# Performance work log

Hardware: AMD Instinct MI355X
Metric: run time of the kernel (lower is better)

Reference implementation:

```python
import jax, jax.numpy as jnp
import numpy as np

BITS = 4
QMAX = 2 ** (BITS - 1) - 1   # 7
OFF = 2 ** (BITS - 1)        # 8
L = 2 ** BITS                # 16 LUT levels per operand


def _quant(x):
    """Symmetric per-tensor quantization to signed BITS-bit levels.
    Returns integer-valued levels (as float, in [-OFF, QMAX]) and the scale."""
    s = jnp.maximum(jnp.max(jnp.abs(x)) / QMAX, 1e-8)
    q = jnp.clip(jnp.round(x / s), -OFF, QMAX)
    return q, s


def _lut_conv3x3(x, w, b, lut):
    """3x3 same-padding conv where every scalar multiply a*w is replaced by
    lut[idx(a), idx(w)]. x:[B,C,H,W], w:[O,C,3,3], b:[O], lut:[L,L]."""
    B, C, H, W = x.shape
    O = w.shape[0]
    qx, sx = _quant(x)
    qw, sw = _quant(w)
    # zero-padding: level 0 is the quantized value 0, so padding is exact
    xp = jnp.pad(qx, ((0, 0), (0, 0), (1, 1), (1, 1)))
    # im2col: [B, C, 9, H, W] -> [B, H, W, K], K = C*9 (order: c-major, then kh,kw)
    patches = jnp.stack([xp[:, :, i:i + H, j:j + W]
                         for i in range(3) for j in range(3)], axis=2)
    K = C * 9
    patches = patches.reshape(B, K, H, W).transpose(0, 2, 3, 1)
    idx_a = (patches + OFF).astype(jnp.int32)            # [B,H,W,K]
    mapped = lut[idx_a]                                   # [B,H,W,K,L]
    idx_w = (qw.reshape(O, K).T + OFF).astype(jnp.int32)  # [K,O]
    onehot_w = jax.nn.one_hot(idx_w, L, dtype=x.dtype)    # [K,O,L]
    # out[b,o,h,w] = sum_k lut[idx_a[b,h,w,k], idx_w[k,o]]
    out = jnp.einsum('bhwkl,kol->bohw', mapped, onehot_w)
    return out * (sx * sw) + b[None, :, None, None]


def _lut_linear(x, w, b, lut):
    """x:[B,F], w:[O,F], b:[O], lut:[L,L]; y[b,o]=sum_f lut[idx(x),idx(w)]."""
    qx, sx = _quant(x)
    qw, sw = _quant(w)
    idx_a = (qx + OFF).astype(jnp.int32)                 # [B,F]
    mapped = lut[idx_a]                                   # [B,F,L]
    idx_w = (qw.T + OFF).astype(jnp.int32)                # [F,O]
    onehot_w = jax.nn.one_hot(idx_w, L, dtype=x.dtype)    # [F,O,L]
    out = jnp.einsum('bfl,fol->bo', mapped, onehot_w)
    return out * (sx * sw) + b[None, :]


def _maxpool2(x):
    B, C, H, W = x.shape
    return x.reshape(B, C, H // 2, 2, W // 2, 2).max(axis=(3, 5))


def setup_inputs() -> dict:
    key = jax.random.key(0)
    ks = jax.random.split(key, 20)
    d = {}
    d['x'] = jax.random.normal(ks[0], (8, 3, 32, 32), jnp.float32)
    conv_shapes = [(64, 3), (192, 64), (384, 192), (256, 384), (256, 256)]
    for i, (o, c) in enumerate(conv_shapes):
        d[f'w{i}'] = jax.random.normal(ks[1 + 2 * i], (o, c, 3, 3), jnp.float32) * 0.05
        d[f'b{i}'] = jax.random.normal(ks[2 + 2 * i], (o,), jnp.float32) * 0.01
    fc_shapes = [(4096, 4096), (4096, 4096), (10, 4096)]
    for j, (o, f) in enumerate(fc_shapes):
        d[f'w{5 + j}'] = jax.random.normal(ks[11 + 2 * j], (o, f), jnp.float32) * 0.02
        d[f'b{5 + j}'] = jax.random.normal(ks[12 + 2 * j], (o,), jnp.float32) * 0.01
    # per-layer approximate-multiplier LUTs: exact product of signed levels + error
    levels = jnp.arange(-OFF, OFF, dtype=jnp.float32)       # [-8..7]
    base = jnp.outer(levels, levels)                        # [16,16]
    noise = jax.random.normal(ks[17], (8, L, L), jnp.float32) * 0.25
    d['luts'] = base[None, :, :] + noise
    return d


def reference(x, w0, b0, w1, b1, w2, b2, w3, b3, w4, b4,
              w5, b5, w6, b6, w7, b7, luts):
    relu = jax.nn.relu
    h = relu(_lut_conv3x3(x, w0, b0, luts[0]))
    h = _maxpool2(h)                                  # [B,64,16,16]
    h = relu(_lut_conv3x3(h, w1, b1, luts[1]))
    h = _maxpool2(h)                                  # [B,192,8,8]
    h = relu(_lut_conv3x3(h, w2, b2, luts[2]))        # [B,384,8,8]
    h = relu(_lut_conv3x3(h, w3, b3, luts[3]))        # [B,256,8,8]
    h = relu(_lut_conv3x3(h, w4, b4, luts[4]))
    h = _maxpool2(h)                                  # [B,256,4,4]
    h = h.reshape(h.shape[0], 256 * 4 * 4)
    h = relu(_lut_linear(h, w5, b5, luts[5]))         # dropout = identity (eval)
    h = relu(_lut_linear(h, w6, b6, luts[6]))
    return _lut_linear(h, w7, b7, luts[7])            # [B,10]
```

## Files before the change

kernel.cpp:

```cpp
#include <hip/hip_runtime.h>
#include <stdint.h>


#define DI __device__ __forceinline__

constexpr size_t alup(size_t x){ return (x + 511) & ~(size_t)511; }
constexpr size_t O_SLOTS = 0;
constexpr size_t O_IA0 = 512;
constexpr size_t O_IA1 = alup(O_IA0 + 24576);
constexpr size_t O_IA2 = alup(O_IA1 + 131072);
constexpr size_t O_IA3 = alup(O_IA2 + 98304);
constexpr size_t O_IA4 = alup(O_IA3 + 196608);
constexpr size_t O_IA5 = alup(O_IA4 + 131072);
constexpr size_t O_IA6 = alup(O_IA5 + 32768);
constexpr size_t O_IA7 = alup(O_IA6 + 32768);
constexpr size_t O_WP0 = alup(O_IA7 + 32768);
constexpr size_t O_WP1 = alup(O_WP0 + 864);
constexpr size_t O_WP2 = alup(O_WP1 + 55296);
constexpr size_t O_WP3 = alup(O_WP2 + 331776);
constexpr size_t O_WP4 = alup(O_WP3 + 442368);
constexpr size_t O_A1  = alup(O_WP4 + 294912);
constexpr size_t O_A2  = alup(O_A1 + 1048576);
constexpr size_t O_A3  = alup(O_A2 + 786432);
constexpr size_t O_A4  = alup(O_A3 + 1572864);
constexpr size_t O_A5  = alup(O_A4 + 1048576);
constexpr size_t O_H5  = alup(O_A5 + 262144);
constexpr size_t O_H6  = alup(O_H5 + 262144);
constexpr size_t O_P1  = alup(O_H6 + 262144);
constexpr size_t O_P2  = O_P1 + 3145728;
constexpr size_t O_P3  = O_P2 + 1572864;
constexpr size_t O_P4  = O_P3 + 1048576;
constexpr int    PZ_D4 = 212992;


DI double getscale(const double* slots, int i){ return fmax(slots[i] / 7.0, 1e-8); }
DI int quant_idx_r(double v, double r){
  double q = fmin(fmax(rint(v * r), -8.0), 7.0);
  return (int)q + 8;
}
DI void atomicMaxD(double* addr, double v){
  atomicMax((unsigned long long*)addr, (unsigned long long)__double_as_longlong(v));
}

__global__ __launch_bounds__(256) void k_zero_all(double4* pz, double* slots){
  int i = blockIdx.x*256 + threadIdx.x;
  if (i < PZ_D4){ double4 z; z.x=z.y=z.z=z.w=0.0; pz[i] = z; }
  else if (i - PZ_D4 < 16) slots[i - PZ_D4] = 0.0;
}

__global__ __launch_bounds__(256) void k_wmax(
    const float* w0, const float* w1, const float* w2, const float* w3, const float* w4,
    const float* w5, const float* w6, const float* w7, const float* x, double* slots)
{
  const int sizes[9] = {1728,110592,663552,884736,589824,16777216,16777216,40960,24576};
  const int cum[10]  = {0,1,5,26,53,71,583,1095,1097,1098};
  int bid = blockIdx.x;
  int seg = 0;
  #pragma unroll
  for (int s2 = 0; s2 < 9; ++s2) if (bid >= cum[s2+1]) seg = s2+1;
  const float* p;
  switch (seg){
    case 0: p = w0; break; case 1: p = w1; break; case 2: p = w2; break;
    case 3: p = w3; break; case 4: p = w4; break; case 5: p = w5; break;
    case 6: p = w6; break; case 7: p = w7; break; default: p = x; break;
  }
  int n = sizes[seg];
  long base = (long)(bid - cum[seg]) * 32768;
  float m = 0.f;
  for (long i = base + threadIdx.x * 4; i < base + 32768 && i < (long)n; i += 1024){
    float4 v = *(const float4*)(p + i);
    m = fmaxf(m, fmaxf(fmaxf(fabsf(v.x), fabsf(v.y)), fmaxf(fabsf(v.z), fabsf(v.w))));
  }
  #pragma unroll
  for (int off = 32; off; off >>= 1) m = fmaxf(m, __shfl_xor(m, off, 64));
  __shared__ float red[4];
  if ((threadIdx.x & 63) == 0) red[threadIdx.x >> 6] = m;
  __syncthreads();
  if (threadIdx.x == 0)
    atomicMaxD(&slots[seg], (double)fmaxf(fmaxf(red[0], red[1]), fmaxf(red[2], red[3])));
}

__global__ __launch_bounds__(256) void k_wq(
    const float* w0, const float* w1, const float* w2, const float* w3, const float* w4,
    const float* x, const double* slots, uint8_t* ws)
{
  int item = blockIdx.x * 256 + threadIdx.x;
  if (item < 281304){
    const float* w; uint32_t* wp; int K; int r; double s;
    if (item < 216)        { w=w0; wp=(uint32_t*)(ws+O_WP0); K=27;   r=item;        s=getscale(slots,0); }
    else if (item < 14040) { w=w1; wp=(uint32_t*)(ws+O_WP1); K=576;  r=item-216;    s=getscale(slots,1); }
    else if (item < 96984) { w=w2; wp=(uint32_t*)(ws+O_WP2); K=1728; r=item-14040;  s=getscale(slots,2); }
    else if (item < 207576){ w=w3; wp=(uint32_t*)(ws+O_WP3); K=3456; r=item-96984;  s=getscale(slots,3); }
    else                   { w=w4; wp=(uint32_t*)(ws+O_WP4); K=2304; r=item-207576; s=getscale(slots,4); }
    double rs = 1.0 / s;
    int og = r / K, k = r % K;
    uint32_t pack = 0;
    #pragma unroll
    for (int j = 0; j < 8; ++j){
      double wv = (double)w[(size_t)(og*8 + j)*K + k];
      pack |= (uint32_t)quant_idx_r(wv, rs) << (4*j);
    }
    wp[og*K + k] = pack;
  } else if (item < 287448){
    int i2 = item - 281304;
    double rs = 1.0 / getscale(slots, 8);
    uint32_t pack = 0;
    #pragma unroll
    for (int r2 = 0; r2 < 4; ++r2)
      pack |= (uint32_t)quant_idx_r((double)x[i2*4 + r2], rs) << (8*r2);
    ((uint32_t*)(ws + O_IA0))[i2] = pack;
  }
}

__global__ __launch_bounds__(256) void k_conv0(
    const uint8_t* __restrict__ ia0, const uint32_t* __restrict__ wp0,
    const float* __restrict__ lut_g, const float* __restrict__ bias,
    double* slots, double* __restrict__ a1)
{
  __shared__ double lutT[256];
  int tid = threadIdx.x;
  lutT[(tid & 15)*16 + (tid >> 4)] = (double)lut_g[tid];
  __syncthreads();
  int b = blockIdx.x >> 6, o = blockIdx.x & 63;
  int yp = tid >> 4, xp = tid & 15;
  double scale = getscale(slots, 8) * getscale(slots, 0);
  double bo = (double)bias[o];
  double pool = 0.0;
  #pragma unroll
  for (int dy = 0; dy < 2; ++dy)
  #pragma unroll
  for (int dx = 0; dx < 2; ++dx){
    int y = yp*2 + dy, x2 = xp*2 + dx;
    double sum = 0.0;
    #pragma unroll
    for (int c = 0; c < 3; ++c)
      #pragma unroll
      for (int ty = 0; ty < 3; ++ty)
        #pragma unroll
        for (int tx = 0; tx < 3; ++tx){
          int yy = y + ty - 1, xx = x2 + tx - 1;
          int ia = 8;
          if (yy >= 0 && yy < 32 && xx >= 0 && xx < 32)
            ia = ia0[((b*3 + c)*32 + yy)*32 + xx];
          uint32_t sw = wp0[(o >> 3)*27 + c*9 + ty*3 + tx];
          int iw = (sw >> ((o & 7)*4)) & 15;
          sum += lutT[iw*16 + ia];
        }
    pool = fmax(pool, fmax(sum*scale + bo, 0.0));
  }
  a1[((b*64 + o)*16 + yp)*16 + xp] = pool;
  double m = pool;
  #pragma unroll
  for (int off = 32; off; off >>= 1) m = fmax(m, __shfl_xor(m, off, 64));
  __shared__ double red[4];
  if ((tid & 63) == 0) red[tid >> 6] = m;
  __syncthreads();
  if (tid == 0) atomicMaxD(&slots[9], fmax(fmax(red[0],red[1]), fmax(red[2],red[3])));
}

template<int C, int O, int H, int W, int CT, int ROWS, int SP, int KS>
__global__ __launch_bounds__(256) void k_conv(
    const uint8_t* __restrict__ iain, const uint32_t* __restrict__ wp,
    const float* __restrict__ lut_g, double* __restrict__ P)
{
  constexpr int KT = CT*9;
  constexpr int AW = W + 2, AH = ROWS + 2;
  __shared__ double lutT[256];
  __shared__ uint32_t wps[4*KT];
  __shared__ uint8_t acts[CT*AH*AW];
  int tid = threadIdx.x;
  int bx = blockIdx.x;
  int ks = bx % KS; int rem = bx / KS;
  int ob = rem % (O/32); rem /= (O/32);
  int sp = rem % SP; int b = rem / SP;
  lutT[(tid & 15)*16 + (tid >> 4)] = (double)lut_g[tid];
  for (int i = tid; i < 4*KT; i += 256){
    int w2 = i / KT, k = i % KT;
    wps[i] = wp[(size_t)(ob*4 + w2)*(C*9) + (size_t)ks*KT + k];
  }
  for (int i = tid; i < CT*AH*AW; i += 256){
    int ct = i / (AH*AW);
    int r  = (i / AW) % AH;
    int cc = i % AW;
    int y = sp*ROWS + r - 1, x2 = cc - 1;
    uint8_t v = 8;
    if (y >= 0 && y < H && x2 >= 0 && x2 < W)
      v = iain[(((size_t)b*C + ks*CT + ct)*H + y)*W + x2];
    acts[i] = v;
  }
  __syncthreads();
  int wid = tid >> 6, lane = tid & 63;
  int ly = lane / W, lx = lane % W;
  double acc[8] = {0,0,0,0,0,0,0,0};
  const uint32_t* wrow = &wps[wid*KT];
  #pragma unroll 1
  for (int ct = 0; ct < CT; ++ct){
    int abase = (ct*AH + ly)*AW + lx;
    #pragma unroll
    for (int ty = 0; ty < 3; ++ty)
    #pragma unroll
    for (int tx = 0; tx < 3; ++tx){
      int ia = acts[abase + ty*AW + tx];
      uint32_t sw = (uint32_t)__builtin_amdgcn_readfirstlane((int)wrow[ct*9 + ty*3 + tx]);
      #pragma unroll
      for (int j = 0; j < 8; ++j)
        acc[j] += lutT[((sw >> (4*j)) & 15u)*16 + ia];
    }
  }
  int y = sp*ROWS + ly;
  int obase = ob*32 + wid*8;
  #pragma unroll
  for (int j = 0; j < 8; ++j)
    atomicAdd(&P[(((size_t)b*O + obase + j)*H + y)*W + lx], acc[j]);
}

template<int O, int Hc, int Wc, bool POOL>
__global__ __launch_bounds__(256) void k_post(
    const double* __restrict__ P, const float* __restrict__ bias,
    double* __restrict__ aout, double* slots, int sx_slot, int sw_slot, int ma_slot)
{
  constexpr int Ho = POOL ? Hc/2 : Hc, Wo = POOL ? Wc/2 : Wc;
  int i = blockIdx.x*256 + threadIdx.x;
  int x2 = i % Wo, y = (i / Wo) % Ho, o = (i / (Wo*Ho)) % O, b = i / (Wo*Ho*O);
  double scale = getscale(slots, sx_slot) * getscale(slots, sw_slot);
  double bo = (double)bias[o];
  double res;
  if (POOL){
    double p = 0.0;
    #pragma unroll
    for (int dy = 0; dy < 2; ++dy)
    #pragma unroll
    for (int dx = 0; dx < 2; ++dx){
      double s = P[(((size_t)b*O + o)*Hc + y*2+dy)*Wc + x2*2+dx];
      p = fmax(p, fmax(s*scale + bo, 0.0));
    }
    res = p;
  } else {
    double s = P[(((size_t)b*O + o)*Hc + y)*Wc + x2];
    res = fmax(s*scale + bo, 0.0);
  }
  aout[i] = res;
  double m = res;
  #pragma unroll
  for (int off = 32; off; off >>= 1) m = fmax(m, __shfl_xor(m, off, 64));
  __shared__ double red[4];
  if ((threadIdx.x & 63) == 0) red[threadIdx.x >> 6] = m;
  __syncthreads();
  if (threadIdx.x == 0)
    atomicMaxD(&slots[ma_slot], fmax(fmax(red[0],red[1]), fmax(red[2],red[3])));
}

__global__ __launch_bounds__(256) void k_aq_conv(
    const double* __restrict__ in, uint8_t* __restrict__ out,
    const double* slots, int slot, int n)
{
  int i = blockIdx.x*256 + threadIdx.x;
  if (i >= n) return;
  double rs = 1.0 / getscale(slots, slot);
  out[i] = (uint8_t)quant_idx_r(in[i], rs);
}

__global__ __launch_bounds__(256) void k_aq_fc(
    const double* __restrict__ in, uint32_t* __restrict__ lo, uint32_t* __restrict__ hi,
    const double* slots, int slot)
{
  int f = blockIdx.x*256 + threadIdx.x;
  double rs = 1.0 / getscale(slots, slot);
  uint32_t l = 0, h = 0;
  #pragma unroll
  for (int b2 = 0; b2 < 4; ++b2) l |= (uint32_t)quant_idx_r(in[(size_t)b2*4096 + f], rs) << (8*b2);
  #pragma unroll
  for (int b2 = 4; b2 < 8; ++b2) h |= (uint32_t)quant_idx_r(in[(size_t)b2*4096 + f], rs) << (8*(b2-4));
  lo[f] = l; hi[f] = h;
}

template<bool RELU>
__global__ __launch_bounds__(256) void k_fc(
    const float* __restrict__ Wm, const float* __restrict__ bias,
    const uint32_t* __restrict__ ialo, const uint32_t* __restrict__ iahi,
    const float* __restrict__ lut_g, double* __restrict__ out,
    double* slots, int sx_slot, int sw_slot, int ma_slot)
{
  __shared__ double lutT[256];
  __shared__ uint32_t los[4096], his[4096];
  __shared__ double red[4];
  int tid = threadIdx.x;
  lutT[(tid & 15)*16 + (tid >> 4)] = (double)lut_g[tid];
  for (int i = tid; i < 4096; i += 256){ los[i] = ialo[i]; his[i] = iahi[i]; }
  __syncthreads();
  double sw = getscale(slots, sw_slot);
  double rsw = 1.0 / sw;
  double scale = getscale(slots, sx_slot) * sw;
  int wid = tid >> 6, lane = tid & 63;
  int o = blockIdx.x*4 + wid;
  const float* wr = Wm + (size_t)o*4096;
  double acc[8] = {0,0,0,0,0,0,0,0};
  #pragma unroll 2
  for (int ch = 0; ch < 64; ++ch){
    int f = ch*64 + lane;
    unsigned iw = (unsigned)quant_idx_r((double)wr[f], rsw);
    const double* lrow = &lutT[iw << 4];
    uint32_t lo = los[f], hi = his[f];
    acc[0] += lrow[lo & 255];         acc[1] += lrow[(lo >> 8) & 255];
    acc[2] += lrow[(lo >> 16) & 255]; acc[3] += lrow[lo >> 24];
    acc[4] += lrow[hi & 255];         acc[5] += lrow[(hi >> 8) & 255];
    acc[6] += lrow[(hi >> 16) & 255]; acc[7] += lrow[hi >> 24];
  }
  #pragma unroll
  for (int off = 32; off; off >>= 1)
    #pragma unroll
    for (int b2 = 0; b2 < 8; ++b2) acc[b2] += __shfl_xor(acc[b2], off, 64);
  if (lane == 0){
    double m = 0.0;
    double bo = (double)bias[o];
    #pragma unroll
    for (int b2 = 0; b2 < 8; ++b2){
      double h = acc[b2]*scale + bo;
      if (RELU) h = fmax(h, 0.0);
      out[(size_t)b2*4096 + o] = h;
      m = fmax(m, fabs(h));
    }
    red[wid] = m;
  }
  __syncthreads();
  if (tid == 0)
    atomicMaxD(&slots[ma_slot], fmax(fmax(red[0],red[1]), fmax(red[2],red[3])));
}

__global__ __launch_bounds__(256) void k_fc7(
    const float* __restrict__ Wm, const float* __restrict__ bias,
    const uint32_t* __restrict__ ialo, const uint32_t* __restrict__ iahi,
    const float* __restrict__ lut_g, float* __restrict__ out, const double* slots)
{
  __shared__ double lutT[256];
  __shared__ uint32_t los[4096], his[4096];
  __shared__ double red[4][8];
  int tid = threadIdx.x;
  lutT[(tid & 15)*16 + (tid >> 4)] = (double)lut_g[tid];
  for (int i = tid; i < 4096; i += 256){ los[i] = ialo[i]; his[i] = iahi[i]; }
  __syncthreads();
  double sw = getscale(slots, 7);
  double rsw = 1.0 / sw;
  double scale = getscale(slots, 15) * sw;
  int o = blockIdx.x;
  const float* wr = Wm + (size_t)o*4096;
  double acc[8] = {0,0,0,0,0,0,0,0};
  for (int ch = 0; ch < 16; ++ch){
    int f = ch*256 + tid;
    unsigned iw = (unsigned)quant_idx_r((double)wr[f], rsw);
    const double* lrow = &lutT[iw << 4];
    uint32_t lo = los[f], hi = his[f];
    acc[0] += lrow[lo & 255];         acc[1] += lrow[(lo >> 8) & 255];
    acc[2] += lrow[(lo >> 16) & 255]; acc[3] += lrow[lo >> 24];
    acc[4] += lrow[hi & 255];         acc[5] += lrow[(hi >> 8) & 255];
    acc[6] += lrow[(hi >> 16) & 255]; acc[7] += lrow[hi >> 24];
  }
  int wid = tid >> 6, lane = tid & 63;
  #pragma unroll
  for (int off = 32; off; off >>= 1)
    #pragma unroll
    for (int b2 = 0; b2 < 8; ++b2) acc[b2] += __shfl_xor(acc[b2], off, 64);
  if (lane == 0){
    #pragma unroll
    for (int b2 = 0; b2 < 8; ++b2) red[wid][b2] = acc[b2];
  }
  __syncthreads();
  if (tid < 8){
    double v = red[0][tid] + red[1][tid] + red[2][tid] + red[3][tid];
    out[tid*10 + o] = (float)(v*scale + (double)bias[o]);
  }
}

extern "C" void kernel_launch(void* const* d_in, const int* in_sizes, int n_in,
                              void* d_out, int out_size, void* d_ws, size_t ws_size,
                              hipStream_t stream)
{
  (void)in_sizes; (void)n_in; (void)out_size; (void)ws_size;
  const float* x  = (const float*)d_in[0];
  const float* w0 = (const float*)d_in[1];  const float* b0 = (const float*)d_in[2];
  const float* w1 = (const float*)d_in[3];  const float* b1 = (const float*)d_in[4];
  const float* w2 = (const float*)d_in[5];  const float* b2 = (const float*)d_in[6];
  const float* w3 = (const float*)d_in[7];  const float* b3 = (const float*)d_in[8];
  const float* w4 = (const float*)d_in[9];  const float* b4 = (const float*)d_in[10];
  const float* w5 = (const float*)d_in[11]; const float* b5 = (const float*)d_in[12];
  const float* w6 = (const float*)d_in[13]; const float* b6 = (const float*)d_in[14];
  const float* w7 = (const float*)d_in[15]; const float* b7 = (const float*)d_in[16];
  const float* luts = (const float*)d_in[17];

  uint8_t* ws = (uint8_t*)d_ws;
  double* slots = (double*)(ws + O_SLOTS);
  const uint8_t* IA0 = ws + O_IA0;
  uint8_t *IA1 = ws + O_IA1, *IA2 = ws + O_IA2, *IA3 = ws + O_IA3, *IA4 = ws + O_IA4;
  uint32_t *IA5lo = (uint32_t*)(ws + O_IA5), *IA5hi = IA5lo + 4096;
  uint32_t *IA6lo = (uint32_t*)(ws + O_IA6), *IA6hi = IA6lo + 4096;
  uint32_t *IA7lo = (uint32_t*)(ws + O_IA7), *IA7hi = IA7lo + 4096;
  const uint32_t* WP0 = (const uint32_t*)(ws + O_WP0);
  const uint32_t* WP1 = (const uint32_t*)(ws + O_WP1);
  const uint32_t* WP2 = (const uint32_t*)(ws + O_WP2);
  const uint32_t* WP3 = (const uint32_t*)(ws + O_WP3);
  const uint32_t* WP4 = (const uint32_t*)(ws + O_WP4);
  double *A1 = (double*)(ws + O_A1), *A2 = (double*)(ws + O_A2), *A3 = (double*)(ws + O_A3);
  double *A4 = (double*)(ws + O_A4), *A5 = (double*)(ws + O_A5);
  double *H5 = (double*)(ws + O_H5), *H6 = (double*)(ws + O_H6);
  double *P1 = (double*)(ws + O_P1), *P2 = (double*)(ws + O_P2);
  double *P3 = (double*)(ws + O_P3), *P4 = (double*)(ws + O_P4);

  k_zero_all<<<833, 256, 0, stream>>>((double4*)(ws + O_P1), slots);
  k_wmax<<<1098, 256, 0, stream>>>(w0,w1,w2,w3,w4,w5,w6,w7,x,slots);
  k_wq<<<1123, 256, 0, stream>>>(w0,w1,w2,w3,w4,x,slots,ws);

  k_conv0<<<512, 256, 0, stream>>>(IA0, WP0, luts + 0, b0, slots, A1);
  k_aq_conv<<<512, 256, 0, stream>>>(A1, IA1, slots, 9, 131072);

  k_conv<64,192,16,16,8,4,4,8><<<1536, 256, 0, stream>>>(IA1, WP1, luts + 256, P1);
  k_post<192,16,16,true><<<384, 256, 0, stream>>>(P1, b1, A2, slots, 9, 1, 10);
  k_aq_conv<<<384, 256, 0, stream>>>(A2, IA2, slots, 10, 98304);

  k_conv<192,384,8,8,12,8,1,16><<<1536, 256, 0, stream>>>(IA2, WP2, luts + 512, P2);
  k_post<384,8,8,false><<<768, 256, 0, stream>>>(P2, b2, A3, slots, 10, 2, 11);
  k_aq_conv<<<768, 256, 0, stream>>>(A3, IA3, slots, 11, 196608);

  k_conv<384,256,8,8,12,8,1,32><<<2048, 256, 0, stream>>>(IA3, WP3, luts + 768, P3);
  k_post<256,8,8,false><<<512, 256, 0, stream>>>(P3, b3, A4, slots, 11, 3, 12);
  k_aq_conv<<<512, 256, 0, stream>>>(A4, IA4, slots, 12, 131072);

  k_conv<256,256,8,8,8,8,1,32><<<2048, 256, 0, stream>>>(IA4, WP4, luts + 1024, P4);
  k_post<256,8,8,true><<<128, 256, 0, stream>>>(P4, b4, A5, slots, 12, 4, 13);
  k_aq_fc<<<16, 256, 0, stream>>>(A5, IA5lo, IA5hi, slots, 13);

  k_fc<true><<<1024, 256, 0, stream>>>(w5, b5, IA5lo, IA5hi, luts + 1280, H5, slots, 13, 5, 14);
  k_aq_fc<<<16, 256, 0, stream>>>(H5, IA6lo, IA6hi, slots, 14);
  k_fc<true><<<1024, 256, 0, stream>>>(w6, b6, IA6lo, IA6hi, luts + 1536, H6, slots, 14, 6, 15);
  k_aq_fc<<<16, 256, 0, stream>>>(H6, IA7lo, IA7hi, slots, 15);
  k_fc7<<<10, 256, 0, stream>>>(w7, b7, IA7lo, IA7hi, luts + 1792, (float*)d_out, slots);
}
```

Before: 503.0 us.

## Fuse activation quantization into conv kernels and process batch pairs with pair LUT

Removes the separate activation-quantization kernels by quantizing the double activations on the fly inside each conv block. Each block now covers 8 output channels across all batch elements, with two batch samples packed into one byte. A 4096-entry float2 pair table serves both samples with one LDS read, and it is indexed through an XOR encoding so two samples with the same level share an entry. conv0 also stages its input tile in shared memory. The catch is that every conv block builds a 32KB shared table and re-quantizes overlapping input, and the LUT values are now accumulated from float rather than double.

```diff
diff --git a/kernel.cpp b/kernel.cpp
--- a/kernel.cpp
+++ b/kernel.cpp
@@ -7,11 +7,7 @@
 constexpr size_t alup(size_t x){ return (x + 511) & ~(size_t)511; }
 constexpr size_t O_SLOTS = 0;
 constexpr size_t O_IA0 = 512;
-constexpr size_t O_IA1 = alup(O_IA0 + 24576);
-constexpr size_t O_IA2 = alup(O_IA1 + 131072);
-constexpr size_t O_IA3 = alup(O_IA2 + 98304);
-constexpr size_t O_IA4 = alup(O_IA3 + 196608);
-constexpr size_t O_IA5 = alup(O_IA4 + 131072);
+constexpr size_t O_IA5 = alup(O_IA0 + 24576);
 constexpr size_t O_IA6 = alup(O_IA5 + 32768);
 constexpr size_t O_IA7 = alup(O_IA6 + 32768);
 constexpr size_t O_WP0 = alup(O_IA7 + 32768);
@@ -118,10 +114,12 @@
     double* slots, double* __restrict__ a1)
 {
   __shared__ double lutT[256];
+  __shared__ uint8_t xs[3072];
   int tid = threadIdx.x;
   lutT[(tid & 15)*16 + (tid >> 4)] = (double)lut_g[tid];
-  __syncthreads();
   int b = blockIdx.x >> 6, o = blockIdx.x & 63;
+  for (int i = tid; i < 3072; i += 256) xs[i] = ia0[b*3072 + i];
+  __syncthreads();
   int yp = tid >> 4, xp = tid & 15;
   double scale = getscale(slots, 8) * getscale(slots, 0);
   double bo = (double)bias[o];
@@ -141,7 +139,7 @@
           int yy = y + ty - 1, xx = x2 + tx - 1;
           int ia = 8;
           if (yy >= 0 && yy < 32 && xx >= 0 && xx < 32)
-            ia = ia0[((b*3 + c)*32 + yy)*32 + xx];
+            ia = xs[(c*32 + yy)*32 + xx];
           uint32_t sw = wp0[(o >> 3)*27 + c*9 + ty*3 + tx];
           int iw = (sw >> ((o & 7)*4)) & 15;
           sum += lutT[iw*16 + ia];
@@ -159,59 +157,75 @@
 }
 
 template<int C, int O, int H, int W, int CT, int ROWS, int SP, int KS>
-__global__ __launch_bounds__(256) void k_conv(
-    const uint8_t* __restrict__ iain, const uint32_t* __restrict__ wp,
-    const float* __restrict__ lut_g, double* __restrict__ P)
+__global__ __launch_bounds__(256) void k_convQ(
+    const double* __restrict__ Ain, const uint32_t* __restrict__ wp,
+    const float* __restrict__ lut_g, const double* __restrict__ slots, int slot,
+    double* __restrict__ P)
 {
   constexpr int KT = CT*9;
   constexpr int AW = W + 2, AH = ROWS + 2;
-  __shared__ double lutT[256];
-  __shared__ uint32_t wps[4*KT];
-  __shared__ uint8_t acts[CT*AH*AW];
+  __shared__ float2 pairT[4096];
+  __shared__ uint32_t wps[KT];
+  __shared__ uint8_t actsC[4*CT*AH*AW];
   int tid = threadIdx.x;
   int bx = blockIdx.x;
   int ks = bx % KS; int rem = bx / KS;
-  int ob = rem % (O/32); rem /= (O/32);
-  int sp = rem % SP; int b = rem / SP;
-  lutT[(tid & 15)*16 + (tid >> 4)] = (double)lut_g[tid];
-  for (int i = tid; i < 4*KT; i += 256){
-    int w2 = i / KT, k = i % KT;
-    wps[i] = wp[(size_t)(ob*4 + w2)*(C*9) + (size_t)ks*KT + k];
-  }
-  for (int i = tid; i < CT*AH*AW; i += 256){
-    int ct = i / (AH*AW);
-    int r  = (i / AW) % AH;
-    int cc = i % AW;
+  int ob = rem % (O/8); int sp = rem / (O/8);
+  for (int e = tid; e < 4096; e += 256){
+    int iw = e >> 8, s8 = e & 255;
+    int a1 = s8 >> 4, a2 = (s8 & 15) ^ a1;
+    pairT[e] = make_float2(lut_g[a1*16 + iw], lut_g[a2*16 + iw]);
+  }
+  for (int i = tid; i < KT; i += 256)
+    wps[i] = wp[(size_t)ob*(C*9) + ks*KT + i];
+  double rs = 1.0 / getscale(slots, slot);
+  constexpr int ATOT = 4*CT*AH*AW;
+  for (int i = tid; i < ATOT; i += 256){
+    int p2 = i / (CT*AH*AW);
+    int r2 = i % (CT*AH*AW);
+    int ct = r2 / (AH*AW);
+    int r = (r2 / AW) % AH;
+    int cc = r2 % AW;
     int y = sp*ROWS + r - 1, x2 = cc - 1;
-    uint8_t v = 8;
-    if (y >= 0 && y < H && x2 >= 0 && x2 < W)
-      v = iain[(((size_t)b*C + ks*CT + ct)*H + y)*W + x2];
-    acts[i] = v;
-  }
-  __syncthreads();
-  int wid = tid >> 6, lane = tid & 63;
+    uint8_t v = 136;
+    if (y >= 0 && y < H && x2 >= 0 && x2 < W){
+      size_t base = ((size_t)(2*p2)*C + ks*CT + ct)*H*W + (size_t)y*W + x2;
+      int q1 = quant_idx_r(Ain[base], rs);
+      int q2 = quant_idx_r(Ain[base + (size_t)C*H*W], rs);
+      v = (uint8_t)((q1 << 4) | q2);
+    }
+    actsC[i] = v;
+  }
+  __syncthreads();
+  int p = tid >> 6, lane = tid & 63;
   int ly = lane / W, lx = lane % W;
-  double acc[8] = {0,0,0,0,0,0,0,0};
-  const uint32_t* wrow = &wps[wid*KT];
+  double acc0[8] = {0,0,0,0,0,0,0,0};
+  double acc1[8] = {0,0,0,0,0,0,0,0};
   #pragma unroll 1
   for (int ct = 0; ct < CT; ++ct){
-    int abase = (ct*AH + ly)*AW + lx;
+    int abase = ((p*CT + ct)*AH + ly)*AW + lx;
     #pragma unroll
     for (int ty = 0; ty < 3; ++ty)
     #pragma unroll
     for (int tx = 0; tx < 3; ++tx){
-      int ia = acts[abase + ty*AW + tx];
-      uint32_t sw = (uint32_t)__builtin_amdgcn_readfirstlane((int)wrow[ct*9 + ty*3 + tx]);
+      int c = actsC[abase + ty*AW + tx];
+      int sl = c ^ (c >> 4);
+      uint32_t sw = (uint32_t)__builtin_amdgcn_readfirstlane((int)wps[ct*9 + ty*3 + tx]);
       #pragma unroll
-      for (int j = 0; j < 8; ++j)
-        acc[j] += lutT[((sw >> (4*j)) & 15u)*16 + ia];
+      for (int j = 0; j < 8; ++j){
+        float2 v = pairT[(((sw >> (4*j)) & 15u) << 8) + sl];
+        acc0[j] += (double)v.x;
+        acc1[j] += (double)v.y;
+      }
     }
   }
   int y = sp*ROWS + ly;
-  int obase = ob*32 + wid*8;
-  #pragma unroll
-  for (int j = 0; j < 8; ++j)
-    atomicAdd(&P[(((size_t)b*O + obase + j)*H + y)*W + lx], acc[j]);
+  #pragma unroll
+  for (int j = 0; j < 8; ++j){
+    size_t base = (((size_t)(2*p)*O + ob*8 + j)*H + y)*W + lx;
+    atomicAdd(&P[base], acc0[j]);
+    atomicAdd(&P[base + (size_t)O*H*W], acc1[j]);
+  }
 }
 
 template<int O, int Hc, int Wc, bool POOL>
@@ -248,16 +262,6 @@
   __syncthreads();
   if (threadIdx.x == 0)
     atomicMaxD(&slots[ma_slot], fmax(fmax(red[0],red[1]), fmax(red[2],red[3])));
-}
-
-__global__ __launch_bounds__(256) void k_aq_conv(
-    const double* __restrict__ in, uint8_t* __restrict__ out,
-    const double* slots, int slot, int n)
-{
-  int i = blockIdx.x*256 + threadIdx.x;
-  if (i >= n) return;
-  double rs = 1.0 / getscale(slots, slot);
-  out[i] = (uint8_t)quant_idx_r(in[i], rs);
 }
 
 __global__ __launch_bounds__(256) void k_aq_fc(
@@ -390,7 +394,6 @@
   uint8_t* ws = (uint8_t*)d_ws;
   double* slots = (double*)(ws + O_SLOTS);
   const uint8_t* IA0 = ws + O_IA0;
-  uint8_t *IA1 = ws + O_IA1, *IA2 = ws + O_IA2, *IA3 = ws + O_IA3, *IA4 = ws + O_IA4;
   uint32_t *IA5lo = (uint32_t*)(ws + O_IA5), *IA5hi = IA5lo + 4096;
   uint32_t *IA6lo = (uint32_t*)(ws + O_IA6), *IA6hi = IA6lo + 4096;
   uint32_t *IA7lo = (uint32_t*)(ws + O_IA7), *IA7hi = IA7lo + 4096;
@@ -410,21 +413,17 @@
   k_wq<<<1123, 256, 0, stream>>>(w0,w1,w2,w3,w4,x,slots,ws);
 
   k_conv0<<<512, 256, 0, stream>>>(IA0, WP0, luts + 0, b0, slots, A1);
-  k_aq_conv<<<512, 256, 0, stream>>>(A1, IA1, slots, 9, 131072);
-
-  k_conv<64,192,16,16,8,4,4,8><<<1536, 256, 0, stream>>>(IA1, WP1, luts + 256, P1);
+
+  k_convQ<64,192,16,16,4,4,4,16><<<1536, 256, 0, stream>>>(A1, WP1, luts + 256, slots, 9, P1);
   k_post<192,16,16,true><<<384, 256, 0, stream>>>(P1, b1, A2, slots, 9, 1, 10);
-  k_aq_conv<<<384, 256, 0, stream>>>(A2, IA2, slots, 10, 98304);
-
-  k_conv<192,384,8,8,12,8,1,16><<<1536, 256, 0, stream>>>(IA2, WP2, luts + 512, P2);
+
+  k_convQ<192,384,8,8,6,8,1,32><<<1536, 256, 0, stream>>>(A2, WP2, luts + 512, slots, 10, P2);
   k_post<384,8,8,false><<<768, 256, 0, stream>>>(P2, b2, A3, slots, 10, 2, 11);
-  k_aq_conv<<<768, 256, 0, stream>>>(A3, IA3, slots, 11, 196608);
-
-  k_conv<384,256,8,8,12,8,1,32><<<2048, 256, 0, stream>>>(IA3, WP3, luts + 768, P3);
+
+  k_convQ<384,256,8,8,8,8,1,48><<<1536, 256, 0, stream>>>(A3, WP3, luts + 768, slots, 11, P3);
   k_post<256,8,8,false><<<512, 256, 0, stream>>>(P3, b3, A4, slots, 11, 3, 12);
-  k_aq_conv<<<512, 256, 0, stream>>>(A4, IA4, slots, 12, 131072);
-
-  k_conv<256,256,8,8,8,8,1,32><<<2048, 256, 0, stream>>>(IA4, WP4, luts + 1024, P4);
+
+  k_convQ<256,256,8,8,4,8,1,64><<<2048, 256, 0, stream>>>(A4, WP4, luts + 1024, slots, 12, P4);
   k_post<256,8,8,true><<<128, 256, 0, stream>>>(P4, b4, A5, slots, 12, 4, 13);
   k_aq_fc<<<16, 256, 0, stream>>>(A5, IA5lo, IA5hi, slots, 13);
 
```

Measured after the change: 651.5 us. 29.5% more time.
